# Optimization experiments

Hardware: AMD Instinct MI355X
Metric: run time of the kernel (lower is better)

The kernel has to match this reference:

```python
import jax, jax.numpy as jnp
import numpy as np

N_NODES = 100000
N_EDGES = 1600000
N_FEAT = 128
HIDDEN = 128
N_CLASSES = 40
MAX_DEPTH = 4
INIT_TEMP = 1.0  # temperature (non-trainable)
N_AGGR = 3       # ['mean', 'max', 'self']


def setup_inputs() -> dict:
    key = jax.random.key(0)
    ks = jax.random.split(key, 16)
    s = 1.0 / np.sqrt(HIDDEN)
    inp = {
        'x': jax.random.normal(ks[0], (N_NODES, N_FEAT), dtype=jnp.float32),
        'edge_index': jax.random.randint(ks[1], (2, N_EDGES), 0, N_NODES, dtype=jnp.int32),
        'W_pre': jax.random.normal(ks[2], (N_FEAT, HIDDEN), dtype=jnp.float32) / np.sqrt(N_FEAT),
        'b_pre': jnp.zeros((HIDDEN,), dtype=jnp.float32),
        'W_depth': jax.random.normal(ks[3], (HIDDEN, 2), dtype=jnp.float32) * s,
        'b_depth': jnp.zeros((2,), dtype=jnp.float32),
        'W_aggr': jax.random.normal(ks[4], (HIDDEN, N_AGGR), dtype=jnp.float32) * s,
        'b_aggr': jnp.zeros((N_AGGR,), dtype=jnp.float32),
        'W_conv': jax.random.normal(ks[5], (MAX_DEPTH, HIDDEN, HIDDEN), dtype=jnp.float32) * s,
        'b_conv': jnp.zeros((MAX_DEPTH, HIDDEN), dtype=jnp.float32),
        'W_post': jax.random.normal(ks[6], (HIDDEN, N_CLASSES), dtype=jnp.float32) * s,
        'b_post': jnp.zeros((N_CLASSES,), dtype=jnp.float32),
    }
    return inp


def _mix_aggr_conv(x, src, dst, deg, W, b, aggr_w):
    # MixAggrConvLayer: transform then per-node convex mix of {mean, max, self}
    h = x @ W + b                                   # [N, H]
    msg = h[src]                                    # [E, H] gather
    mean_a = jax.ops.segment_sum(msg, dst, num_segments=N_NODES) / deg[:, None]
    max_a = jax.ops.segment_max(msg, dst, num_segments=N_NODES)
    max_a = jnp.where(jnp.isfinite(max_a), max_a, 0.0)  # isolated nodes -> 0
    return aggr_w[:, 0:1] * mean_a + aggr_w[:, 1:2] * max_a + aggr_w[:, 2:3] * h


def reference(x, edge_index, W_pre, b_pre, W_depth, b_depth, W_aggr, b_aggr,
              W_conv, b_conv, W_post, b_post):
    src, dst = edge_index[0], edge_index[1]
    deg = jnp.maximum(
        jax.ops.segment_sum(jnp.ones((src.shape[0],), jnp.float32), dst,
                            num_segments=N_NODES), 1.0)

    # pre_mp + (Dropout eval = identity) + ReLU
    h = jax.nn.relu(x @ W_pre + b_pre)              # [N, H]

    continue_pr = jnp.ones((N_NODES,), jnp.float32)
    selected = jnp.zeros((N_NODES, HIDDEN), jnp.float32)
    for i in range(MAX_DEPTH):
        hd = jax.lax.stop_gradient(h)               # controllers see detached x
        stop_prob = jax.nn.softmax((hd @ W_depth + b_depth) / INIT_TEMP, axis=-1)
        aggr_prob = jax.nn.softmax((hd @ W_aggr + b_aggr) / INIT_TEMP, axis=-1)
        h = _mix_aggr_conv(h, src, dst, deg, W_conv[i], b_conv[i], aggr_prob)
        h = jax.nn.relu(h)                          # dropout (eval) + relu
        selected = selected + (continue_pr * stop_prob[:, 1])[:, None] * h
        continue_pr = continue_pr * stop_prob[:, 0]

    logits = selected @ W_post + b_post             # [N, C]
    return jax.nn.log_softmax(logits, axis=1)
```

## Files before the change

### kernel.cpp

```cpp
#include <hip/hip_runtime.h>
#include <math.h>

#define HIDDEN 128
#define NCLS 40
#define BMAX 1024

typedef __attribute__((ext_vector_type(8))) short short8;
typedef __attribute__((ext_vector_type(4))) float f32x4;
typedef __attribute__((ext_vector_type(2))) float f32x2;

__device__ __forceinline__ unsigned short f2bf(float f) {
    unsigned u = __float_as_uint(f);
    unsigned r = u + 0x7FFFu + ((u >> 16) & 1u);
    return (unsigned short)(r >> 16);
}
__device__ __forceinline__ float bf_lo(unsigned u) { return __uint_as_float(u << 16); }
__device__ __forceinline__ float bf_hi(unsigned u) { return __uint_as_float(u & 0xFFFF0000u); }

__global__ void k_wprep(const float* __restrict__ Wp, const float* __restrict__ Wc,
                        const float* __restrict__ Wd, const float* __restrict__ Wa,
                        unsigned short* __restrict__ WpreT, unsigned short* __restrict__ WT) {
    int i = blockIdx.x * 256 + threadIdx.x;
    if (i < 16384) {
        int n = i >> 7, k = i & 127;
        WpreT[i] = f2bf(Wp[k * 128 + n]);
    } else if (i < 16384 + 4 * 18432) {
        int j = i - 16384;
        int d = j / 18432;
        int rem = j % 18432;
        int n = rem >> 7, k = rem & 127;
        float v = 0.f;
        if (n < 128)      v = Wc[d * 16384 + k * 128 + n];
        else if (n < 130) v = Wd[k * 2 + (n - 128)];
        else if (n < 133) v = Wa[k * 3 + (n - 130)];
        WT[j] = f2bf(v);
    }
}


__launch_bounds__(256)
__global__ void k_bcount(const int* __restrict__ ei, int E, int* __restrict__ bucket_cnt) {
    __shared__ int hist[BMAX];
    const int tid = threadIdx.x;
    for (int i = tid; i < BMAX; i += 256) hist[i] = 0;
    __syncthreads();
    const int e0 = blockIdx.x * 4096;
    #pragma unroll
    for (int i = 0; i < 16; i++) {
        int e = e0 + i * 256 + tid;
        if (e < E) atomicAdd(&hist[ei[E + e] >> 8], 1);
    }
    __syncthreads();
    for (int i = tid; i < BMAX; i += 256) {
        int v = hist[i];
        if (v > 0) atomicAdd(&bucket_cnt[i], v);
    }
}

__global__ void k_bscan(const int* __restrict__ bucket_cnt, int nb,
                        int* __restrict__ bucket_base, int* __restrict__ bucket_cursor) {
    __shared__ int sd[256];
    const int tid = threadIdx.x;
    int v[4];
    int sum = 0;
    #pragma unroll
    for (int j = 0; j < 4; j++) {
        int b = tid * 4 + j;
        v[j] = (b < nb) ? bucket_cnt[b] : 0;
        sum += v[j];
    }
    sd[tid] = sum;
    __syncthreads();
    #pragma unroll
    for (int off = 1; off < 256; off <<= 1) {
        int t = (tid >= off) ? sd[tid - off] : 0;
        __syncthreads();
        sd[tid] += t;
        __syncthreads();
    }
    int base = sd[tid] - sum;
    #pragma unroll
    for (int j = 0; j < 4; j++) {
        int b = tid * 4 + j;
        if (b < nb) {
            bucket_base[b] = base;
            bucket_cursor[b] = base;
            base += v[j];
        }
    }
}

__launch_bounds__(256)
__global__ void k_bin(const int* __restrict__ ei, int E,
                      int* __restrict__ bucket_cursor, unsigned* __restrict__ binned) {
    __shared__ int hist[BMAX];
    __shared__ int rankc[BMAX];
    __shared__ int lbase[BMAX];
    const int tid = threadIdx.x;
    const int e0 = blockIdx.x * 4096;
    for (int i = tid; i < BMAX; i += 256) { hist[i] = 0; rankc[i] = 0; }
    __syncthreads();
    int bkt[16];
    unsigned pk[16];
    #pragma unroll
    for (int i = 0; i < 16; i++) {
        int e = e0 + i * 256 + tid;
        if (e < E) {
            int s = ei[e];
            int d = ei[E + e];
            bkt[i] = d >> 8;
            pk[i] = ((unsigned)(d & 255) << 24) | (unsigned)s;
            atomicAdd(&hist[bkt[i]], 1);
        } else bkt[i] = -1;
    }
    __syncthreads();
    for (int i = tid; i < BMAX; i += 256)
        if (hist[i] > 0) lbase[i] = atomicAdd(&bucket_cursor[i], hist[i]);
    __syncthreads();
    #pragma unroll
    for (int i = 0; i < 16; i++) {
        if (bkt[i] >= 0) {
            int r = atomicAdd(&rankc[bkt[i]], 1);
            binned[lbase[bkt[i]] + r] = pk[i];
        }
    }
}

__launch_bounds__(256)
__global__ void k_scatter(const unsigned* __restrict__ binned,
                          const int* __restrict__ bucket_base,
                          const int* __restrict__ bucket_cnt,
                          int* __restrict__ row_start, int* __restrict__ deg_i,
                          float* __restrict__ degf,
                          int* __restrict__ csr_off, int N) {
    __shared__ int hist[256];
    __shared__ int rs[256];
    __shared__ int cur[256];
    const int tid = threadIdx.x;
    hist[tid] = 0;
    __syncthreads();
    const int base = bucket_base[blockIdx.x];
    const int cnt = bucket_cnt[blockIdx.x];
    for (int i = tid; i < cnt; i += 256)
        atomicAdd(&hist[binned[base + i] >> 24], 1);
    __syncthreads();
    int v = hist[tid];
    rs[tid] = v;
    __syncthreads();
    #pragma unroll
    for (int off = 1; off < 256; off <<= 1) {
        int t = (tid >= off) ? rs[tid - off] : 0;
        __syncthreads();
        rs[tid] += t;
        __syncthreads();
    }
    int gstart = base + rs[tid] - v;
    int n = (blockIdx.x << 8) + tid;
    if (n < N) {
        row_start[n] = gstart;
        deg_i[n] = v;
        degf[n] = fmaxf((float)v, 1.0f);
    }
    __syncthreads();
    rs[tid] = gstart;
    cur[tid] = 0;
    __syncthreads();
    for (int i = tid; i < cnt; i += 256) {
        unsigned p = binned[base + i];
        int dl = (int)(p >> 24);
        int r = atomicAdd(&cur[dl], 1);
        csr_off[rs[dl] + r] = (int)((p & 0xFFFFFFu) << 7);
    }
}


template <bool AF32, bool CTRL>
__launch_bounds__(256)
__global__ void k_gemm_mfma(const void* __restrict__ Ain,
                            const unsigned short* __restrict__ Wt,
                            const float* __restrict__ bias,
                            unsigned short* __restrict__ Cb,
                            unsigned char* __restrict__ C8,
                            float* __restrict__ ctrl,
                            int M, int do_relu) {
    __shared__ unsigned short Ws[144 * 132];
    const int tid = threadIdx.x;
    const int lane = tid & 63;
    const int wv = tid >> 6;
    const int row_blk = blockIdx.x * 128;
    const int rows0 = wv * 32;
    const int l15 = lane & 15;
    const int q = lane >> 4;
    const int RWS = CTRL ? 144 : 128;

    for (int c = tid; c < RWS * 16; c += 256) {
        int r = c >> 4, ch = c & 15;
        *(uint4*)&Ws[r * 132 + ch * 8] = *(const uint4*)(Wt + (size_t)r * HIDDEN + ch * 8);
    }
    __syncthreads();

    f32x4 acc[2][8] = {};
    f32x4 acc5[2] = {};
    for (int k0 = 0; k0 < 128; k0 += 32) {
        short8 af[2];
        #pragma unroll
        for (int mi = 0; mi < 2; mi++) {
            int ar = row_blk + rows0 + mi * 16 + l15;
            if (AF32) {
                const float* A = (const float*)Ain;
                float4 v0 = make_float4(0.f, 0.f, 0.f, 0.f);
                float4 v1 = make_float4(0.f, 0.f, 0.f, 0.f);
                if (ar < M) {
                    v0 = *(const float4*)(A + (size_t)ar * HIDDEN + k0 + q * 8);
                    v1 = *(const float4*)(A + (size_t)ar * HIDDEN + k0 + q * 8 + 4);
                }
                short8 t;
                t[0] = (short)f2bf(v0.x); t[1] = (short)f2bf(v0.y);
                t[2] = (short)f2bf(v0.z); t[3] = (short)f2bf(v0.w);
                t[4] = (short)f2bf(v1.x); t[5] = (short)f2bf(v1.y);
                t[6] = (short)f2bf(v1.z); t[7] = (short)f2bf(v1.w);
                af[mi] = t;
            } else {
                const unsigned short* A = (const unsigned short*)Ain;
                short8 t = {};
                if (ar < M) t = *(const short8*)(A + (size_t)ar * HIDDEN + k0 + q * 8);
                af[mi] = t;
            }
        }
        #pragma unroll
        for (int ni = 0; ni < 8; ni++) {
            short8 bw = *(const short8*)&Ws[(ni * 16 + l15) * 132 + k0 + q * 8];
            #pragma unroll
            for (int mi = 0; mi < 2; mi++)
                acc[mi][ni] = __builtin_amdgcn_mfma_f32_16x16x32_bf16(
                    bw, af[mi], acc[mi][ni], 0, 0, 0);
        }
        if (CTRL) {
            short8 bc = *(const short8*)&Ws[(128 + l15) * 132 + k0 + q * 8];
            #pragma unroll
            for (int mi = 0; mi < 2; mi++)
                acc5[mi] = __builtin_amdgcn_mfma_f32_16x16x32_bf16(
                    bc, af[mi], acc5[mi], 0, 0, 0);
        }
    }
    #pragma unroll
    for (int mi = 0; mi < 2; mi++) {
        int node = row_blk + rows0 + mi * 16 + l15;
        if (node < M) {
            #pragma unroll
            for (int ni = 0; ni < 8; ni++) {
                int fb = ni * 16 + q * 4;
                float4 bv = *(const float4*)&bias[fb];
                float o0 = acc[mi][ni][0] + bv.x;
                float o1 = acc[mi][ni][1] + bv.y;
                float o2 = acc[mi][ni][2] + bv.z;
                float o3 = acc[mi][ni][3] + bv.w;
                if (do_relu) {
                    o0 = fmaxf(o0, 0.f); o1 = fmaxf(o1, 0.f);
                    o2 = fmaxf(o2, 0.f); o3 = fmaxf(o3, 0.f);
                }
                ushort4 ov;
                ov.x = f2bf(o0); ov.y = f2bf(o1); ov.z = f2bf(o2); ov.w = f2bf(o3);
                *(ushort4*)(Cb + (size_t)node * HIDDEN + fb) = ov;
                if (CTRL) {
                    unsigned w8 = 0;
                    w8 = __builtin_amdgcn_cvt_pk_fp8_f32(o0, o1, w8, 0);
                    w8 = __builtin_amdgcn_cvt_pk_fp8_f32(o2, o3, w8, 1);
                    *(unsigned*)(C8 + (size_t)node * HIDDEN + fb) = w8;
                }
            }
            if (CTRL) {
                if (q == 0) {
                    *(float4*)(ctrl + (size_t)node * 8) =
                        make_float4(acc5[mi][0], acc5[mi][1], acc5[mi][2], acc5[mi][3]);
                } else if (q == 1) {
                    ctrl[(size_t)node * 8 + 4] = acc5[mi][0];
                }
            }
        }
    }
}


__launch_bounds__(256)
__global__ void k_depth(const unsigned char* __restrict__ ht8,
                        const unsigned short* __restrict__ ht,
                        unsigned short* __restrict__ h_out,
                        float* __restrict__ cp, float* __restrict__ wsel,
                        const float* __restrict__ ctrl,
                        const float* __restrict__ degf, const int* __restrict__ deg_i,
                        const int* __restrict__ row_start, const int* __restrict__ csr_off,
                        const float* __restrict__ bd, const float* __restrict__ ba,
                        int N, int first) {
    const int lane = threadIdx.x & 63;
    const int wave = threadIdx.x >> 6;
    const int node = blockIdx.x * 4 + wave;
    if (node >= N) return;
    const int nodeu = __builtin_amdgcn_readfirstlane(node);
    const int half = lane >> 5;
    const int fb = (lane & 31) * 4;
    const int f8 = fb;
    const char* htb = (const char*)ht;

    float4 c4 = *(const float4*)(ctrl + (size_t)nodeu * 8);
    float cl4 = ctrl[(size_t)nodeu * 8 + 4];
    float d0 = c4.x + bd[0], d1 = c4.y + bd[1];
    float a0 = c4.z + ba[0], a1 = c4.w + ba[1], a2 = cl4 + ba[2];
    float m2 = fmaxf(d0, d1);
    float e0 = __expf(d0 - m2), e1 = __expf(d1 - m2);
    float inv2 = 1.f / (e0 + e1);
    float sp0 = e0 * inv2, sp1 = e1 * inv2;
    float m3 = fmaxf(fmaxf(a0, a1), a2);
    float f0 = __expf(a0 - m3), f1 = __expf(a1 - m3), f2 = __expf(a2 - m3);
    float inv3 = 1.f / (f0 + f1 + f2);
    float ap0 = f0 * inv3, ap1 = f1 * inv3, ap2 = f2 * inv3;

    const int cnt = deg_i[nodeu];
    const int start = row_start[nodeu];
    const float invd = 1.0f / degf[nodeu];

    float s0 = 0.f, s1 = 0.f, s2 = 0.f, s3 = 0.f;
    float x0m = -3.4e38f, x1m = -3.4e38f, x2m = -3.4e38f, x3m = -3.4e38f;

    for (int eb = 0; eb < cnt; eb += 64) {
        int idx = eb + lane;
        int soff = (idx < cnt) ? csr_off[start + idx] : 0;
        int lim = min(64, cnt - eb);
        int lim2 = lim & ~1;
        int j = 0;
        #define GPAIR(JJ)                                                     \
        {                                                                     \
            int o = __shfl(soff, (JJ) + half);                                \
            unsigned u = *(const unsigned*)(ht8 + (unsigned)(o + f8));        \
            f32x2 plo = __builtin_amdgcn_cvt_pk_f32_fp8(u, 0);                \
            f32x2 phi = __builtin_amdgcn_cvt_pk_f32_fp8(u, 1);                \
            s0 += plo.x; s1 += plo.y; s2 += phi.x; s3 += phi.y;               \
            x0m = fmaxf(x0m, plo.x); x1m = fmaxf(x1m, plo.y);                 \
            x2m = fmaxf(x2m, phi.x); x3m = fmaxf(x3m, phi.y);                 \
        }
        for (; j + 16 <= lim2; j += 16) {
            GPAIR(j) GPAIR(j + 2) GPAIR(j + 4) GPAIR(j + 6)
            GPAIR(j + 8) GPAIR(j + 10) GPAIR(j + 12) GPAIR(j + 14)
        }
        for (; j + 4 <= lim2; j += 4) { GPAIR(j) GPAIR(j + 2) }
        for (; j < lim2; j += 2) GPAIR(j)
        #undef GPAIR
        if (lim & 1) {
            int o = __shfl(soff, lim - 1);
            if (half == 0) {
                unsigned u = *(const unsigned*)(ht8 + (unsigned)(o + f8));
                f32x2 plo = __builtin_amdgcn_cvt_pk_f32_fp8(u, 0);
                f32x2 phi = __builtin_amdgcn_cvt_pk_f32_fp8(u, 1);
                s0 += plo.x; s1 += plo.y; s2 += phi.x; s3 += phi.y;
                x0m = fmaxf(x0m, plo.x); x1m = fmaxf(x1m, plo.y);
                x2m = fmaxf(x2m, phi.x); x3m = fmaxf(x3m, phi.y);
            }
        }
    }
    s0 += __shfl_xor(s0, 32); s1 += __shfl_xor(s1, 32);
    s2 += __shfl_xor(s2, 32); s3 += __shfl_xor(s3, 32);
    x0m = fmaxf(x0m, __shfl_xor(x0m, 32)); x1m = fmaxf(x1m, __shfl_xor(x1m, 32));
    x2m = fmaxf(x2m, __shfl_xor(x2m, 32)); x3m = fmaxf(x3m, __shfl_xor(x3m, 32));

    if (cnt == 0) { x0m = 0.f; x1m = 0.f; x2m = 0.f; x3m = 0.f; }

    if (half == 0) {
        uint2 su = *(const uint2*)(htb + (unsigned)(nodeu * 256 + fb * 2));
        float h0 = ap0 * (s0 * invd) + ap1 * x0m + ap2 * bf_lo(su.x);
        float h1 = ap0 * (s1 * invd) + ap1 * x1m + ap2 * bf_hi(su.x);
        float h2 = ap0 * (s2 * invd) + ap1 * x2m + ap2 * bf_lo(su.y);
        float h3 = ap0 * (s3 * invd) + ap1 * x3m + ap2 * bf_hi(su.y);
        h0 = fmaxf(h0, 0.f); h1 = fmaxf(h1, 0.f);
        h2 = fmaxf(h2, 0.f); h3 = fmaxf(h3, 0.f);
        ushort4 ho;
        ho.x = f2bf(h0); ho.y = f2bf(h1); ho.z = f2bf(h2); ho.w = f2bf(h3);
        *(ushort4*)(h_out + (size_t)nodeu * HIDDEN + fb) = ho;
    }
    if (lane == 0) {
        float cpv = first ? 1.0f : cp[nodeu];
        wsel[nodeu] = cpv * sp1;
        cp[nodeu] = cpv * sp0;
    }
}


__launch_bounds__(256)
__global__ void k_post(const unsigned short* __restrict__ h_all, size_t hstride,
                       const float* __restrict__ wsel, int N,
                       const float* __restrict__ Wp, const float* __restrict__ bp,
                       float* __restrict__ out) {
    __shared__ float Ss[32][132];
    __shared__ float Wt[NCLS][132];
    __shared__ float bs[NCLS];
    const int tid = threadIdx.x;
    const int n0 = blockIdx.x * 32;

    for (int i = tid; i < (HIDDEN * NCLS) / 4; i += 256) {
        float4 v = *(const float4*)&Wp[i * 4];
        int f = i * 4;
        int k = f / NCLS, c = f % NCLS;
        float e[4] = {v.x, v.y, v.z, v.w};
        #pragma unroll
        for (int j = 0; j < 4; j++) {
            int cc = c + j, kk = k;
            if (cc >= NCLS) { cc -= NCLS; kk++; }
            Wt[cc][kk] = e[j];
        }
    }
    if (tid < NCLS) bs[tid] = bp[tid];

    const int node_l = tid >> 3;
    const int kc = (tid & 7) * 16;
    const int ng = n0 + node_l;
    float sel[16];
    #pragma unroll
    for (int i = 0; i < 16; i++) sel[i] = 0.f;
    if (ng < N) {
        #pragma unroll
        for (int d = 0; d < 4; d++) {
            float w = wsel[(size_t)d * N + ng];
            const unsigned short* hrow = h_all + (size_t)(d + 1) * hstride + (size_t)ng * HIDDEN;
            #pragma unroll
            for (int u = 0; u < 2; u++) {
                uint4 p = *(const uint4*)(hrow + kc + u * 8);
                unsigned vs[4] = {p.x, p.y, p.z, p.w};
                #pragma unroll
                for (int j = 0; j < 4; j++) {
                    sel[u * 8 + j * 2 + 0] += w * bf_lo(vs[j]);
                    sel[u * 8 + j * 2 + 1] += w * bf_hi(vs[j]);
                }
            }
        }
    }
    #pragma unroll
    for (int u = 0; u < 4; u++)
        *(float4*)&Ss[node_l][kc + u * 4] =
            make_float4(sel[u * 4], sel[u * 4 + 1], sel[u * 4 + 2], sel[u * 4 + 3]);
    __syncthreads();

    const int c0 = (tid & 7) * 5;
    float z[5];
    #pragma unroll
    for (int i = 0; i < 5; i++) z[i] = bs[c0 + i];
    for (int k = 0; k < HIDDEN; k += 4) {
        float4 s4 = *(const float4*)&Ss[node_l][k];
        #pragma unroll
        for (int i = 0; i < 5; i++) {
            float4 w4 = *(const float4*)&Wt[c0 + i][k];
            z[i] += s4.x * w4.x + s4.y * w4.y + s4.z * w4.z + s4.w * w4.w;
        }
    }
    float m = z[0];
    #pragma unroll
    for (int i = 1; i < 5; i++) m = fmaxf(m, z[i]);
    #pragma unroll
    for (int off = 1; off < 8; off <<= 1) m = fmaxf(m, __shfl_xor(m, off));
    float s = 0.f;
    #pragma unroll
    for (int i = 0; i < 5; i++) s += expf(z[i] - m);
    #pragma unroll
    for (int off = 1; off < 8; off <<= 1) s += __shfl_xor(s, off);
    float lg = m + logf(s);
    if (ng < N) {
        #pragma unroll
        for (int i = 0; i < 5; i++)
            out[(size_t)ng * NCLS + c0 + i] = z[i] - lg;
    }
}


extern "C" void kernel_launch(void* const* d_in, const int* in_sizes, int n_in,
                              void* d_out, int out_size, void* d_ws, size_t ws_size,
                              hipStream_t stream) {
    const float* x      = (const float*)d_in[0];
    const int*   ei     = (const int*)d_in[1];
    const float* W_pre  = (const float*)d_in[2];
    const float* b_pre  = (const float*)d_in[3];
    const float* W_dep  = (const float*)d_in[4];
    const float* b_dep  = (const float*)d_in[5];
    const float* W_aggr = (const float*)d_in[6];
    const float* b_aggr = (const float*)d_in[7];
    const float* W_conv = (const float*)d_in[8];
    const float* b_conv = (const float*)d_in[9];
    const float* W_post = (const float*)d_in[10];
    const float* b_post = (const float*)d_in[11];

    const int N = in_sizes[0] / HIDDEN;
    const int E = in_sizes[1] / 2;
    const int nbuckets = (N + 255) >> 8;

    char* ws = (char*)d_ws;
    size_t off = 0;
    auto alloc = [&](size_t bytes) -> void* {
        void* p = ws + off;
        off += (bytes + 255) & ~(size_t)255;
        return p;
    };
    const size_t hstride = (size_t)N * HIDDEN;
    unsigned short* h_all  = (unsigned short*)alloc(5 * hstride * 2);
    unsigned short* ht     = (unsigned short*)alloc(hstride * 2);
    unsigned char*  ht8    = (unsigned char*)alloc(hstride);
    float* cp       = (float*)alloc((size_t)N * 4);
    float* wsel     = (float*)alloc((size_t)4 * N * 4);
    float* degf     = (float*)alloc((size_t)N * 4);
    float* ctrl     = (float*)alloc((size_t)N * 8 * 4);
    unsigned short* WpreT = (unsigned short*)alloc(128 * 128 * 2);
    unsigned short* WT    = (unsigned short*)alloc(4 * 144 * 128 * 2);
    int*   deg_i    = (int*)alloc((size_t)N * 4);
    int*   row_start= (int*)alloc((size_t)N * 4);
    int*   bucket_cnt    = (int*)alloc(BMAX * 4);
    int*   bucket_base   = (int*)alloc(BMAX * 4);
    int*   bucket_cursor = (int*)alloc(BMAX * 4);
    int*   csr_off  = (int*)alloc((size_t)E * 4);
    unsigned* binned = (unsigned*)alloc((size_t)E * 4);

    hipMemsetAsync(bucket_cnt, 0, BMAX * 4, stream);

    int ebb = (E + 4095) / 4096;
    k_bcount<<<ebb, 256, 0, stream>>>(ei, E, bucket_cnt);
    k_bscan<<<1, 256, 0, stream>>>(bucket_cnt, nbuckets, bucket_base, bucket_cursor);
    k_bin<<<ebb, 256, 0, stream>>>(ei, E, bucket_cursor, binned);
    k_scatter<<<nbuckets, 256, 0, stream>>>(binned, bucket_base, bucket_cnt,
                                            row_start, deg_i, degf, csr_off, N);

    int wtot = 16384 + 4 * 18432;
    k_wprep<<<(wtot + 255) / 256, 256, 0, stream>>>(W_pre, W_conv, W_dep, W_aggr,
                                                    WpreT, WT);

    int gblk = (N + 127) / 128;
    k_gemm_mfma<true, false><<<gblk, 256, 0, stream>>>(x, WpreT, b_pre, h_all,
                                                       nullptr, nullptr, N, 1);

    int nb4 = (N + 3) / 4;
    for (int d = 0; d < 4; d++) {
        unsigned short* h_d  = h_all + (size_t)d * hstride;
        unsigned short* h_n  = h_all + (size_t)(d + 1) * hstride;
        k_gemm_mfma<false, true><<<gblk, 256, 0, stream>>>(h_d, WT + (size_t)d * 18432,
                                                           b_conv + (size_t)d * HIDDEN,
                                                           ht, ht8, ctrl, N, 0);
        k_depth<<<nb4, 256, 0, stream>>>(ht8, ht, h_n, cp, wsel + (size_t)d * N, ctrl,
                                         degf, deg_i, row_start, csr_off,
                                         b_dep, b_aggr, N, d == 0 ? 1 : 0);
    }
    k_post<<<(N + 31) / 32, 256, 0, stream>>>(h_all, hstride, wsel, N,
                                              W_post, b_post, (float*)d_out);
}
```

Measured before the change: 551.0 us.

## Remap depth aggregation to one edge per step with two features per lane

The per-node aggregation kernel now has each of the 64 lanes own two features and walk edges one at a time. Edge offsets are broadcast with readlane instead of shuffles, which removes the half-wave split and the final cross-half shuffle reduction. Index and self-row loads are issued earlier, the inverse degree is computed from the integer count, and reciprocal intrinsics replace divisions. The GEMM epilogue also uses the packed hardware bf16 conversion instruction. The trade-off is narrower 2-byte gathers per lane and twice as many serial edge iterations per wave.

```diff
diff --git a/kernel.cpp b/kernel.cpp
--- a/kernel.cpp
+++ b/kernel.cpp
@@ -259,9 +259,12 @@
                     o0 = fmaxf(o0, 0.f); o1 = fmaxf(o1, 0.f);
                     o2 = fmaxf(o2, 0.f); o3 = fmaxf(o3, 0.f);
                 }
-                ushort4 ov;
-                ov.x = f2bf(o0); ov.y = f2bf(o1); ov.z = f2bf(o2); ov.w = f2bf(o3);
-                *(ushort4*)(Cb + (size_t)node * HIDDEN + fb) = ov;
+                unsigned plo, phi;
+                asm("v_cvt_pk_bf16_f32 %0, %1, %2" : "=v"(plo) : "v"(o0), "v"(o1));
+                asm("v_cvt_pk_bf16_f32 %0, %1, %2" : "=v"(phi) : "v"(o2), "v"(o3));
+                uint2 ov;
+                ov.x = plo; ov.y = phi;
+                *(uint2*)(Cb + (size_t)node * HIDDEN + fb) = ov;
                 if (CTRL) {
                     unsigned w8 = 0;
                     w8 = __builtin_amdgcn_cvt_pk_fp8_f32(o0, o1, w8, 0);
@@ -288,7 +291,7 @@
                         unsigned short* __restrict__ h_out,
                         float* __restrict__ cp, float* __restrict__ wsel,
                         const float* __restrict__ ctrl,
-                        const float* __restrict__ degf, const int* __restrict__ deg_i,
+                        const int* __restrict__ deg_i,
                         const int* __restrict__ row_start, const int* __restrict__ csr_off,
                         const float* __restrict__ bd, const float* __restrict__ ba,
                         int N, int first) {
@@ -297,85 +300,69 @@
     const int node = blockIdx.x * 4 + wave;
     if (node >= N) return;
     const int nodeu = __builtin_amdgcn_readfirstlane(node);
-    const int half = lane >> 5;
-    const int fb = (lane & 31) * 4;
-    const int f8 = fb;
-    const char* htb = (const char*)ht;
-
+    const int lane2 = lane << 1;
+
+    const int cnt = deg_i[nodeu];
+    const int start = row_start[nodeu];
+
+    int soff = (lane < cnt) ? csr_off[start + lane] : 0;
+    unsigned su = *(const unsigned*)((const char*)ht + ((size_t)nodeu << 8) + (lane << 2));
     float4 c4 = *(const float4*)(ctrl + (size_t)nodeu * 8);
     float cl4 = ctrl[(size_t)nodeu * 8 + 4];
+
     float d0 = c4.x + bd[0], d1 = c4.y + bd[1];
     float a0 = c4.z + ba[0], a1 = c4.w + ba[1], a2 = cl4 + ba[2];
     float m2 = fmaxf(d0, d1);
     float e0 = __expf(d0 - m2), e1 = __expf(d1 - m2);
-    float inv2 = 1.f / (e0 + e1);
+    float inv2 = __builtin_amdgcn_rcpf(e0 + e1);
     float sp0 = e0 * inv2, sp1 = e1 * inv2;
     float m3 = fmaxf(fmaxf(a0, a1), a2);
     float f0 = __expf(a0 - m3), f1 = __expf(a1 - m3), f2 = __expf(a2 - m3);
-    float inv3 = 1.f / (f0 + f1 + f2);
+    float inv3 = __builtin_amdgcn_rcpf(f0 + f1 + f2);
     float ap0 = f0 * inv3, ap1 = f1 * inv3, ap2 = f2 * inv3;
 
-    const int cnt = deg_i[nodeu];
-    const int start = row_start[nodeu];
-    const float invd = 1.0f / degf[nodeu];
-
-    float s0 = 0.f, s1 = 0.f, s2 = 0.f, s3 = 0.f;
-    float x0m = -3.4e38f, x1m = -3.4e38f, x2m = -3.4e38f, x3m = -3.4e38f;
+    f32x2 sacc = {0.f, 0.f};
+    float mx0 = -3.4e38f, mx1 = -3.4e38f;
+
+    #define EDGE(JJ)                                                          \
+    {                                                                         \
+        int so_ = __builtin_amdgcn_readlane(soff, (JJ));                      \
+        const unsigned char* bp_ = ht8 + (unsigned)so_;                       \
+        unsigned u_ = *(const unsigned short*)(bp_ + lane2);                  \
+        f32x2 p_ = __builtin_amdgcn_cvt_pk_f32_fp8(u_, 0);                    \
+        sacc += p_;                                                           \
+        mx0 = fmaxf(mx0, p_.x); mx1 = fmaxf(mx1, p_.y);                       \
+    }
 
     for (int eb = 0; eb < cnt; eb += 64) {
-        int idx = eb + lane;
-        int soff = (idx < cnt) ? csr_off[start + idx] : 0;
+        if (eb) {
+            int idx = eb + lane;
+            soff = (idx < cnt) ? csr_off[start + idx] : 0;
+        }
         int lim = min(64, cnt - eb);
-        int lim2 = lim & ~1;
         int j = 0;
-        #define GPAIR(JJ)                                                     \
-        {                                                                     \
-            int o = __shfl(soff, (JJ) + half);                                \
-            unsigned u = *(const unsigned*)(ht8 + (unsigned)(o + f8));        \
-            f32x2 plo = __builtin_amdgcn_cvt_pk_f32_fp8(u, 0);                \
-            f32x2 phi = __builtin_amdgcn_cvt_pk_f32_fp8(u, 1);                \
-            s0 += plo.x; s1 += plo.y; s2 += phi.x; s3 += phi.y;               \
-            x0m = fmaxf(x0m, plo.x); x1m = fmaxf(x1m, plo.y);                 \
-            x2m = fmaxf(x2m, phi.x); x3m = fmaxf(x3m, phi.y);                 \
-        }
-        for (; j + 16 <= lim2; j += 16) {
-            GPAIR(j) GPAIR(j + 2) GPAIR(j + 4) GPAIR(j + 6)
-            GPAIR(j + 8) GPAIR(j + 10) GPAIR(j + 12) GPAIR(j + 14)
-        }
-        for (; j + 4 <= lim2; j += 4) { GPAIR(j) GPAIR(j + 2) }
-        for (; j < lim2; j += 2) GPAIR(j)
-        #undef GPAIR
-        if (lim & 1) {
-            int o = __shfl(soff, lim - 1);
-            if (half == 0) {
-                unsigned u = *(const unsigned*)(ht8 + (unsigned)(o + f8));
-                f32x2 plo = __builtin_amdgcn_cvt_pk_f32_fp8(u, 0);
-                f32x2 phi = __builtin_amdgcn_cvt_pk_f32_fp8(u, 1);
-                s0 += plo.x; s1 += plo.y; s2 += phi.x; s3 += phi.y;
-                x0m = fmaxf(x0m, plo.x); x1m = fmaxf(x1m, plo.y);
-                x2m = fmaxf(x2m, phi.x); x3m = fmaxf(x3m, phi.y);
-            }
-        }
-    }
-    s0 += __shfl_xor(s0, 32); s1 += __shfl_xor(s1, 32);
-    s2 += __shfl_xor(s2, 32); s3 += __shfl_xor(s3, 32);
-    x0m = fmaxf(x0m, __shfl_xor(x0m, 32)); x1m = fmaxf(x1m, __shfl_xor(x1m, 32));
-    x2m = fmaxf(x2m, __shfl_xor(x2m, 32)); x3m = fmaxf(x3m, __shfl_xor(x3m, 32));
-
-    if (cnt == 0) { x0m = 0.f; x1m = 0.f; x2m = 0.f; x3m = 0.f; }
-
-    if (half == 0) {
-        uint2 su = *(const uint2*)(htb + (unsigned)(nodeu * 256 + fb * 2));
-        float h0 = ap0 * (s0 * invd) + ap1 * x0m + ap2 * bf_lo(su.x);
-        float h1 = ap0 * (s1 * invd) + ap1 * x1m + ap2 * bf_hi(su.x);
-        float h2 = ap0 * (s2 * invd) + ap1 * x2m + ap2 * bf_lo(su.y);
-        float h3 = ap0 * (s3 * invd) + ap1 * x3m + ap2 * bf_hi(su.y);
-        h0 = fmaxf(h0, 0.f); h1 = fmaxf(h1, 0.f);
-        h2 = fmaxf(h2, 0.f); h3 = fmaxf(h3, 0.f);
-        ushort4 ho;
-        ho.x = f2bf(h0); ho.y = f2bf(h1); ho.z = f2bf(h2); ho.w = f2bf(h3);
-        *(ushort4*)(h_out + (size_t)nodeu * HIDDEN + fb) = ho;
-    }
+        for (; j + 16 <= lim; j += 16) {
+            EDGE(j)      EDGE(j + 1)  EDGE(j + 2)  EDGE(j + 3)
+            EDGE(j + 4)  EDGE(j + 5)  EDGE(j + 6)  EDGE(j + 7)
+            EDGE(j + 8)  EDGE(j + 9)  EDGE(j + 10) EDGE(j + 11)
+            EDGE(j + 12) EDGE(j + 13) EDGE(j + 14) EDGE(j + 15)
+        }
+        for (; j + 4 <= lim; j += 4) {
+            EDGE(j) EDGE(j + 1) EDGE(j + 2) EDGE(j + 3)
+        }
+        for (; j < lim; j++) EDGE(j)
+    }
+    #undef EDGE
+
+    if (cnt == 0) { mx0 = 0.f; mx1 = 0.f; }
+    float invd = __builtin_amdgcn_rcpf(fmaxf((float)cnt, 1.0f));
+    float h0 = ap0 * (sacc.x * invd) + ap1 * mx0 + ap2 * bf_lo(su);
+    float h1 = ap0 * (sacc.y * invd) + ap1 * mx1 + ap2 * bf_hi(su);
+    h0 = fmaxf(h0, 0.f);
+    h1 = fmaxf(h1, 0.f);
+    unsigned po = ((unsigned)f2bf(h1) << 16) | (unsigned)f2bf(h0);
+    *(unsigned*)((char*)h_out + ((size_t)nodeu << 8) + (lane << 2)) = po;
+
     if (lane == 0) {
         float cpv = first ? 1.0f : cp[nodeu];
         wsel[nodeu] = cpv * sp1;
@@ -539,7 +526,7 @@
                                                            b_conv + (size_t)d * HIDDEN,
                                                            ht, ht8, ctrl, N, 0);
         k_depth<<<nb4, 256, 0, stream>>>(ht8, ht, h_n, cp, wsel + (size_t)d * N, ctrl,
-                                         degf, deg_i, row_start, csr_off,
+                                         deg_i, row_start, csr_off,
                                          b_dep, b_aggr, N, d == 0 ? 1 : 0);
     }
     k_post<<<(N + 31) / 32, 256, 0, stream>>>(h_all, hstride, wsel, N,
```

Measured after the change: 531.6 us. -3.5%, faster.
